# Kernel optimization log

Measured on AMD Instinct MI355X. Metric: run time of the kernel, lower is better.

The kernel has to match this reference:

```python
import jax, jax.numpy as jnp
import numpy as np

N = 50000      # nodes
F_IN = 128     # input features
H = 128        # hidden channels
C = 2          # num classes
E = 1600000    # edges
EPS = 1e-5     # BatchNorm eps


def setup_inputs() -> dict:
    key = jax.random.key(0)
    ks = jax.random.split(key, 4)
    x = jax.random.normal(ks[0], (N, F_IN), dtype=jnp.float32)
    edge_index = jax.random.randint(ks[1], (2, E), 0, N, dtype=jnp.int64)
    W1 = jax.random.normal(ks[2], (F_IN, H), dtype=jnp.float32) * 0.05
    W2 = jax.random.normal(ks[3], (H, C), dtype=jnp.float32) * 0.05
    return {
        "x": x, "edge_index": edge_index,
        "bn0_gamma": jnp.ones((F_IN,), jnp.float32), "bn0_beta": jnp.zeros((F_IN,), jnp.float32),
        "bn0_mean": jnp.zeros((F_IN,), jnp.float32), "bn0_var": jnp.ones((F_IN,), jnp.float32),
        "W1": W1, "b1": jnp.zeros((H,), jnp.float32),
        "bn1_gamma": jnp.ones((H,), jnp.float32), "bn1_beta": jnp.zeros((H,), jnp.float32),
        "bn1_mean": jnp.zeros((H,), jnp.float32), "bn1_var": jnp.ones((H,), jnp.float32),
        "W2": W2, "b2": jnp.zeros((C,), jnp.float32),
    }


def batch_norm_eval(x, gamma, beta, mean, var):
    # BatchNorm over nodes, eval mode: use running stats
    return (x - mean) * jax.lax.rsqrt(var + EPS) * gamma + beta


def gcn_conv(x, edge_index, W, b):
    # GCNConv: x @ W, add self-loops, symmetric deg^{-1/2} normalization, scatter-add
    n = x.shape[0]
    xw = x @ W  # [N, out]
    loop = jnp.arange(n, dtype=edge_index.dtype)
    src = jnp.concatenate([edge_index[0], loop])
    dst = jnp.concatenate([edge_index[1], loop])
    deg = jax.ops.segment_sum(jnp.ones_like(dst, dtype=x.dtype), dst, num_segments=n)
    dinv = jnp.where(deg > 0, jax.lax.rsqrt(jnp.maximum(deg, 1.0)), 0.0)
    norm = dinv[src] * dinv[dst]  # [E+N]
    out = jax.ops.segment_sum(xw[src] * norm[:, None], dst, num_segments=n)
    return out + b


def reference(x, edge_index, bn0_gamma, bn0_beta, bn0_mean, bn0_var,
              W1, b1, bn1_gamma, bn1_beta, bn1_mean, bn1_var, W2, b2):
    # Eval mode: dropout / dropout_edge are identity
    h = batch_norm_eval(x, bn0_gamma, bn0_beta, bn0_mean, bn0_var)
    h = gcn_conv(h, edge_index, W1, b1)
    h = batch_norm_eval(h, bn1_gamma, bn1_beta, bn1_mean, bn1_var)
    h = jax.nn.relu(h)
    return gcn_conv(h, edge_index, W2, b2)
```

## Files before the change

kernel.cpp:

```cpp
#include <hip/hip_runtime.h>

#define EPS 1e-5f
#define CAP 128
#define DR  128
#define NB  391
#define CB  4608
#define GS  16
#define CHUNK 4096

typedef __attribute__((ext_vector_type(8))) short bf16x8;
typedef __attribute__((ext_vector_type(4))) float f32x4;

__device__ __forceinline__ unsigned int f2bf(float f) {
  union { float f; unsigned int u; } v; v.f = f;
  return (v.u + 0x7fffu + ((v.u >> 16) & 1u)) >> 16;
}
__device__ __forceinline__ float bf2f_lo(unsigned int u) {
  union { unsigned int i; float f; } v; v.i = u << 16; return v.f;
}
__device__ __forceinline__ float bf2f_hi(unsigned int u) {
  union { unsigned int i; float f; } v; v.i = u & 0xffff0000u; return v.f;
}

__global__ __launch_bounds__(256) void k_A(
    const int* __restrict__ esrc, const int* __restrict__ edst,
    int* __restrict__ gcur, unsigned int* __restrict__ coarse, int e, int nb_p1,
    const float* __restrict__ W1, const float* __restrict__ b1,
    const float* __restrict__ g0, const float* __restrict__ be0,
    const float* __restrict__ m0, const float* __restrict__ v0,
    const float* __restrict__ g1, const float* __restrict__ be1,
    const float* __restrict__ m1, const float* __restrict__ v1,
    const float4* __restrict__ x,
    unsigned short* __restrict__ Wb, float* __restrict__ c1,
    float* __restrict__ s1, float* __restrict__ u1,
    float* __restrict__ dinv, unsigned short* __restrict__ xsb,
    uint2* __restrict__ Xb4, int n, int n4, int npad4) {
  __shared__ int hist[NB];
  __shared__ int base[NB];
  __shared__ int loff[NB];
  __shared__ float s0s[128], t0s[128];
  const int tid = threadIdx.x;
  int bid = blockIdx.x;
  if (bid < nb_p1) {
    for (int i = tid; i < NB; i += 256) { hist[i] = 0; loff[i] = 0; }
    __syncthreads();
    int e0 = bid * CHUNK;
    int e1 = min(e0 + CHUNK, e);
    for (int i = e0 + tid; i < e1; i += 256)
      atomicAdd(&hist[edst[i] >> 7], 1);
    __syncthreads();
    int rot = bid % NB;
    for (int bb = tid; bb < NB; bb += 256) {
      int b = bb + rot; if (b >= NB) b -= NB;
      int h = hist[b];
      if (h > 0) base[b] = atomicAdd(&gcur[b * GS], h);
    }
    __syncthreads();
    for (int i = e0 + tid; i < e1; i += 256) {
      int d = edst[i], s = esrc[i];
      int b = d >> 7;
      int p = base[b] + atomicAdd(&loff[b], 1);
      if (p < CB) coarse[(size_t)b * CB + p] = ((unsigned int)(d & 127) << 16) | (unsigned int)s;
    }
    return;
  }
  if (bid == nb_p1) {
    if (tid < 128) {
      float s0 = g0[tid] * rsqrtf(v0[tid] + EPS);
      s0s[tid] = s0;
      t0s[tid] = be0[tid] - m0[tid] * s0;
      float s = g1[tid] * rsqrtf(v1[tid] + EPS);
      s1[tid] = s;
      u1[tid] = fmaf(b1[tid] - m1[tid], s, be1[tid]);
    }
    __syncthreads();
    if (tid < 128) {
      float acc = 0.f;
      for (int k = 0; k < 128; ++k) acc = fmaf(t0s[k], W1[k * 128 + tid], acc);
      c1[tid] = acc;
    }
    if (tid == 0) dinv[n] = 0.f;
    if (tid < 16) ((uint4*)xsb)[(size_t)n * 16 + tid] = make_uint4(0, 0, 0, 0);
    for (int idx = tid; idx < 16384; idx += 256) {
      int k = idx >> 7, col = idx & 127;
      float w = W1[idx] * s0s[k];
      int c = k >> 5, j = k & 7, lq2 = (k >> 3) & 3;
      int t = col >> 4, li = col & 15;
      Wb[(((c * 8 + t) * 64) + lq2 * 16 + li) * 8 + j] = (unsigned short)f2bf(w);
    }
    return;
  }
  int i = (bid - nb_p1 - 1) * 256 + tid;
  if (i >= npad4) return;
  uint2 o = make_uint2(0u, 0u);
  if (i < n4) {
    float4 v = x[i];
    o.x = (f2bf(v.y) << 16) | f2bf(v.x);
    o.y = (f2bf(v.w) << 16) | f2bf(v.z);
  }
  Xb4[i] = o;
}

__global__ __launch_bounds__(256) void k_B(
    const int* __restrict__ gcur, const unsigned int* __restrict__ coarse,
    unsigned short* __restrict__ slot, int* __restrict__ wcnt, float* __restrict__ dinv,
    const unsigned short* __restrict__ Xb, const unsigned short* __restrict__ Wb,
    const float* __restrict__ c1, unsigned short* __restrict__ xsb, int n) {
  __shared__ int lcnt[DR];
  __shared__ int nqr[DR];
  __shared__ unsigned short lslot[DR * CAP];
  const int tid = threadIdx.x;
  if (blockIdx.x < NB) {
    for (int i = tid; i < DR; i += 256) lcnt[i] = 0;
    unsigned int padpat = ((unsigned int)n << 16) | (unsigned int)n;
    for (int q = tid; q < DR * CAP / 2; q += 256) ((unsigned int*)lslot)[q] = padpat;
    __syncthreads();
    int cb = blockIdx.x;
    int cnt = gcur[cb * GS]; if (cnt > CB) cnt = CB;
    const unsigned int* src = coarse + (size_t)cb * CB;
    for (int i = tid; i < cnt; i += 256) {
      unsigned int v = src[i];
      int ld = (int)(v >> 16);
      int pos = atomicAdd(&lcnt[ld], 1);
      if (pos < CAP) lslot[ld * CAP + pos] = (unsigned short)(v & 0xffffu);
    }
    __syncthreads();
    int dbase = cb * DR;
    for (int ld = tid; ld < DR; ld += 256) {
      int c = min(lcnt[ld], CAP);
      nqr[ld] = ((((c + 3) >> 2) + 3) & ~3);
      int d = dbase + ld;
      if (d < n) {
        wcnt[d] = c;
        dinv[d] = rsqrtf((float)c + 1.0f);
      }
    }
    __syncthreads();
    const uint2* ls8 = (const uint2*)lslot;
    uint2* s8 = (uint2*)slot;
    for (int idx = tid; idx < DR * 32; idx += 256) {
      int ld = idx >> 5, qi = idx & 31;
      if (qi < nqr[ld] && dbase + ld < n) s8[(size_t)cb * (DR * 32) + idx] = ls8[idx];
    }
    return;
  }
  const int gb = blockIdx.x - NB;
  const int wave = tid >> 6, lane = tid & 63;
  const int r0 = gb * 64 + wave * 16;
  const int lr = lane & 15, lq = lane >> 4;
  const bf16x8* a_base = (const bf16x8*)(Xb + (size_t)(r0 + lr) * 128);
  const bf16x8* wb = (const bf16x8*)Wb;
  f32x4 acc[8];
#pragma unroll
  for (int t = 0; t < 8; ++t) acc[t] = (f32x4){0.f, 0.f, 0.f, 0.f};
#pragma unroll
  for (int c = 0; c < 4; ++c) {
    bf16x8 a = a_base[c * 4 + lq];
#pragma unroll
    for (int t = 0; t < 8; ++t) {
      bf16x8 b = wb[(c * 8 + t) * 64 + lane];
      acc[t] = __builtin_amdgcn_mfma_f32_16x16x32_bf16(a, b, acc[t], 0, 0, 0);
    }
  }
#pragma unroll
  for (int reg = 0; reg < 4; ++reg) {
    int row = r0 + lq * 4 + reg;
    if (row < n) {
      unsigned short* orow = xsb + (size_t)row * 128 + lr;
#pragma unroll
      for (int t = 0; t < 8; ++t) {
        float v = acc[t][reg] + c1[t * 16 + lr];
        orow[t * 16] = (unsigned short)f2bf(v);
      }
    }
  }
}

__global__ __launch_bounds__(256) void k_gather1(const int* __restrict__ wcnt,
                                                 const unsigned short* __restrict__ slot,
                                                 const uint4* __restrict__ xs4,
                                                 const float* __restrict__ dinv,
                                                 const float* __restrict__ s1,
                                                 const float* __restrict__ u1,
                                                 const float* __restrict__ W2,
                                                 float* __restrict__ xs2, int n) {
  int wave = threadIdx.x >> 6, lane = threadIdx.x & 63;
  int d = blockIdx.x * 4 + wave;
  if (d >= n) return;
  int sub = lane >> 4, cl = lane & 15;
  int cnt = wcnt[d];
  int nq4 = ((((cnt + 3) >> 2) + 3) & ~3);
  const unsigned short* slotd = slot + ((size_t)d << 7);
  float a0 = 0.f, a1 = 0.f, a2 = 0.f, a3 = 0.f, a4 = 0.f, a5 = 0.f, a6 = 0.f, a7 = 0.f;
#define ACCF(R, DV) { a0 = fmaf(DV, bf2f_lo(R.x), a0); a1 = fmaf(DV, bf2f_hi(R.x), a1); \
                      a2 = fmaf(DV, bf2f_lo(R.y), a2); a3 = fmaf(DV, bf2f_hi(R.y), a3); \
                      a4 = fmaf(DV, bf2f_lo(R.z), a4); a5 = fmaf(DV, bf2f_hi(R.z), a5); \
                      a6 = fmaf(DV, bf2f_lo(R.w), a6); a7 = fmaf(DV, bf2f_hi(R.w), a7); }
  for (int q = 0; q < nq4; q += 4) {
    int i0 = slotd[(q + 0) * 4 + sub];
    int i1 = slotd[(q + 1) * 4 + sub];
    int i2 = slotd[(q + 2) * 4 + sub];
    int i3 = slotd[(q + 3) * 4 + sub];
    float d0 = dinv[i0], d1 = dinv[i1], d2 = dinv[i2], d3 = dinv[i3];
    uint4 r0 = xs4[(size_t)i0 * 16 + cl];
    uint4 r1 = xs4[(size_t)i1 * 16 + cl];
    uint4 r2 = xs4[(size_t)i2 * 16 + cl];
    uint4 r3 = xs4[(size_t)i3 * 16 + cl];
    ACCF(r0, d0); ACCF(r1, d1); ACCF(r2, d2); ACCF(r3, d3);
  }
#define FOLD(OFF) { a0 += __shfl_xor(a0, OFF); a1 += __shfl_xor(a1, OFF); \
                    a2 += __shfl_xor(a2, OFF); a3 += __shfl_xor(a3, OFF); \
                    a4 += __shfl_xor(a4, OFF); a5 += __shfl_xor(a5, OFF); \
                    a6 += __shfl_xor(a6, OFF); a7 += __shfl_xor(a7, OFF); }
  FOLD(16); FOLD(32);
  float dd = dinv[d];
  uint4 sr = xs4[(size_t)d * 16 + cl];
  ACCF(sr, dd);
#undef ACCF
#undef FOLD
  float4 sA = ((const float4*)s1)[cl * 2], sB = ((const float4*)s1)[cl * 2 + 1];
  float4 uA = ((const float4*)u1)[cl * 2], uB = ((const float4*)u1)[cl * 2 + 1];
  float h0 = fmaxf(fmaf(a0 * dd, sA.x, uA.x), 0.f);
  float h1 = fmaxf(fmaf(a1 * dd, sA.y, uA.y), 0.f);
  float h2 = fmaxf(fmaf(a2 * dd, sA.z, uA.z), 0.f);
  float h3 = fmaxf(fmaf(a3 * dd, sA.w, uA.w), 0.f);
  float h4 = fmaxf(fmaf(a4 * dd, sB.x, uB.x), 0.f);
  float h5 = fmaxf(fmaf(a5 * dd, sB.y, uB.y), 0.f);
  float h6 = fmaxf(fmaf(a6 * dd, sB.z, uB.z), 0.f);
  float h7 = fmaxf(fmaf(a7 * dd, sB.w, uB.w), 0.f);
  float4 wA = ((const float4*)W2)[cl * 4 + 0];
  float4 wB = ((const float4*)W2)[cl * 4 + 1];
  float4 wC = ((const float4*)W2)[cl * 4 + 2];
  float4 wD = ((const float4*)W2)[cl * 4 + 3];
  float p0 = h0 * wA.x + h1 * wA.z + h2 * wB.x + h3 * wB.z
           + h4 * wC.x + h5 * wC.z + h6 * wD.x + h7 * wD.z;
  float p1 = h0 * wA.y + h1 * wA.w + h2 * wB.y + h3 * wB.w
           + h4 * wC.y + h5 * wC.w + h6 * wD.y + h7 * wD.w;
  for (int off = 1; off < 16; off <<= 1) {
    p0 += __shfl_xor(p0, off);
    p1 += __shfl_xor(p1, off);
  }
  if (lane == 0) ((float2*)xs2)[d] = make_float2(p0 * dd, p1 * dd);
}

__global__ __launch_bounds__(256) void k_gather2(const int* __restrict__ wcnt,
                                                 const unsigned short* __restrict__ slot,
                                                 const float* __restrict__ xs2,
                                                 const float* __restrict__ dinv,
                                                 const float* __restrict__ b2,
                                                 float* __restrict__ out, int n) {
  int wave = threadIdx.x >> 6, lane = threadIdx.x & 63;
  int d = blockIdx.x * 4 + wave;
  if (d >= n) return;
  int cnt = wcnt[d];
  const unsigned short* slotd = slot + ((size_t)d << 7);
  float p0 = 0.f, p1 = 0.f;
  for (int k = lane; k < cnt; k += 64) {
    int s = slotd[k];
    float2 v = ((const float2*)xs2)[s];
    p0 += v.x; p1 += v.y;
  }
  for (int off = 32; off > 0; off >>= 1) {
    p0 += __shfl_down(p0, off);
    p1 += __shfl_down(p1, off);
  }
  if (lane == 0) {
    float dd = dinv[d];
    float2 self = ((const float2*)xs2)[d];
    out[d * 2 + 0] = fmaf(dd, p0 + self.x, b2[0]);
    out[d * 2 + 1] = fmaf(dd, p1 + self.y, b2[1]);
  }
}

extern "C" void kernel_launch(void* const* d_in, const int* in_sizes, int n_in,
                              void* d_out, int out_size, void* d_ws, size_t ws_size,
                              hipStream_t stream) {
  const float* x   = (const float*)d_in[0];
  const int*   ei  = (const int*)d_in[1];
  const float* g0  = (const float*)d_in[2];
  const float* be0 = (const float*)d_in[3];
  const float* m0  = (const float*)d_in[4];
  const float* v0  = (const float*)d_in[5];
  const float* W1  = (const float*)d_in[6];
  const float* b1  = (const float*)d_in[7];
  const float* g1  = (const float*)d_in[8];
  const float* be1 = (const float*)d_in[9];
  const float* m1  = (const float*)d_in[10];
  const float* v1  = (const float*)d_in[11];
  const float* W2  = (const float*)d_in[12];
  const float* b2  = (const float*)d_in[13];
  float* out = (float*)d_out;

  const int n = in_sizes[0] / 128;
  const int e = in_sizes[1] / 2;
  const int* esrc = ei;
  const int* edst = ei + e;
  const int npad = ((n + 63) / 64) * 64;

  int*            gcur   = (int*)d_ws;
  unsigned int*   coarse = (unsigned int*)(gcur + 6272);
  unsigned short* slot   = (unsigned short*)(coarse + (size_t)NB * CB);
  int*            wcnt   = (int*)(slot + (size_t)n * CAP);
  float*          dinv   = (float*)(wcnt + n);
  unsigned short* Wb     = (unsigned short*)(dinv + n + 4);
  float*          c1     = (float*)(Wb + 16384);
  float*          s1     = c1 + 128;
  float*          u1     = s1 + 128;
  float*          xs2    = u1 + 128;
  unsigned short* Xb     = (unsigned short*)(xs2 + (size_t)n * 2);
  unsigned short* xsb    = Xb + (size_t)npad * 128;

  const int nb_p1 = (e + CHUNK - 1) / CHUNK;
  const int cvb   = (npad * 32 + 255) / 256;
  hipMemsetAsync(gcur, 0, NB * GS * sizeof(int), stream);
  k_A<<<nb_p1 + 1 + cvb, 256, 0, stream>>>(esrc, edst, gcur, coarse, e, nb_p1,
                                           W1, b1, g0, be0, m0, v0, g1, be1, m1, v1,
                                           (const float4*)x, Wb, c1, s1, u1, dinv, xsb,
                                           (uint2*)Xb, n, n * 32, npad * 32);
  k_B<<<NB + npad / 64, 256, 0, stream>>>(gcur, coarse, slot, wcnt, dinv, Xb, Wb, c1, xsb, n);
  k_gather1<<<(n + 3) / 4, 256, 0, stream>>>(wcnt, slot, (const uint4*)xsb, dinv, s1, u1, W2, xs2, n);
  k_gather2<<<(n + 3) / 4, 256, 0, stream>>>(wcnt, slot, xs2, dinv, b2, out, n);
}
```

Baseline: 215.1 us.

## Fuse all GCN stages into one cooperative persistent kernel with grid syncs

Replaces the memset and four separate kernel launches with a single cooperative kernel. The stages are separated by grid.sync, and work is distributed in grid-stride loops over a persistent grid sized from occupancy. It also adds a pass that prescales the bf16 hidden features by dinv, so the gather no longer loads dinv per neighbour, at the cost of an extra read-write sweep and a second bf16 rounding. The aim is to remove launch gaps and per-edge dinv loads. The risks are grid-sync overhead and lower parallelism in the gather stages, since the grid is limited to resident blocks.

```diff
diff --git a/kernel.cpp b/kernel.cpp
--- a/kernel.cpp
+++ b/kernel.cpp
@@ -1,4 +1,5 @@
 #include <hip/hip_runtime.h>
+#include <hip/hip_cooperative_groups.h>
 
 #define EPS 1e-5f
 #define CAP 128
@@ -22,279 +23,270 @@
   union { unsigned int i; float f; } v; v.i = u & 0xffff0000u; return v.f;
 }
 
-__global__ __launch_bounds__(256) void k_A(
-    const int* __restrict__ esrc, const int* __restrict__ edst,
-    int* __restrict__ gcur, unsigned int* __restrict__ coarse, int e, int nb_p1,
-    const float* __restrict__ W1, const float* __restrict__ b1,
-    const float* __restrict__ g0, const float* __restrict__ be0,
-    const float* __restrict__ m0, const float* __restrict__ v0,
-    const float* __restrict__ g1, const float* __restrict__ be1,
-    const float* __restrict__ m1, const float* __restrict__ v1,
-    const float4* __restrict__ x,
-    unsigned short* __restrict__ Wb, float* __restrict__ c1,
-    float* __restrict__ s1, float* __restrict__ u1,
-    float* __restrict__ dinv, unsigned short* __restrict__ xsb,
-    uint2* __restrict__ Xb4, int n, int n4, int npad4) {
-  __shared__ int hist[NB];
-  __shared__ int base[NB];
-  __shared__ int loff[NB];
-  __shared__ float s0s[128], t0s[128];
+struct Params {
+  const int *esrc, *edst;
+  const float4* x;
+  const float *W1, *b1, *g0, *be0, *m0, *v0, *g1, *be1, *m1, *v1, *W2, *b2;
+  int* gcur; unsigned int* coarse; unsigned short* slot; int* wcnt; float* dinv;
+  unsigned short* Wb; float *c1, *s1, *u1, *xs2;
+  unsigned short *Xb, *xsb;
+  float* out;
+  int n, e, npad, nbp1;
+};
+
+__global__ __launch_bounds__(256, 4) void k_fused(Params P) {
+  namespace cg = cooperative_groups;
+  cg::grid_group grid = cg::this_grid();
+  __shared__ int SM[8448];
   const int tid = threadIdx.x;
-  int bid = blockIdx.x;
-  if (bid < nb_p1) {
-    for (int i = tid; i < NB; i += 256) { hist[i] = 0; loff[i] = 0; }
-    __syncthreads();
-    int e0 = bid * CHUNK;
-    int e1 = min(e0 + CHUNK, e);
-    for (int i = e0 + tid; i < e1; i += 256)
-      atomicAdd(&hist[edst[i] >> 7], 1);
-    __syncthreads();
-    int rot = bid % NB;
-    for (int bb = tid; bb < NB; bb += 256) {
-      int b = bb + rot; if (b >= NB) b -= NB;
-      int h = hist[b];
-      if (h > 0) base[b] = atomicAdd(&gcur[b * GS], h);
-    }
-    __syncthreads();
-    for (int i = e0 + tid; i < e1; i += 256) {
-      int d = edst[i], s = esrc[i];
-      int b = d >> 7;
-      int p = base[b] + atomicAdd(&loff[b], 1);
-      if (p < CB) coarse[(size_t)b * CB + p] = ((unsigned int)(d & 127) << 16) | (unsigned int)s;
-    }
-    return;
-  }
-  if (bid == nb_p1) {
-    if (tid < 128) {
-      float s0 = g0[tid] * rsqrtf(v0[tid] + EPS);
-      s0s[tid] = s0;
-      t0s[tid] = be0[tid] - m0[tid] * s0;
-      float s = g1[tid] * rsqrtf(v1[tid] + EPS);
-      s1[tid] = s;
-      u1[tid] = fmaf(b1[tid] - m1[tid], s, be1[tid]);
-    }
-    __syncthreads();
-    if (tid < 128) {
-      float acc = 0.f;
-      for (int k = 0; k < 128; ++k) acc = fmaf(t0s[k], W1[k * 128 + tid], acc);
-      c1[tid] = acc;
-    }
-    if (tid == 0) dinv[n] = 0.f;
-    if (tid < 16) ((uint4*)xsb)[(size_t)n * 16 + tid] = make_uint4(0, 0, 0, 0);
-    for (int idx = tid; idx < 16384; idx += 256) {
-      int k = idx >> 7, col = idx & 127;
-      float w = W1[idx] * s0s[k];
-      int c = k >> 5, j = k & 7, lq2 = (k >> 3) & 3;
-      int t = col >> 4, li = col & 15;
-      Wb[(((c * 8 + t) * 64) + lq2 * 16 + li) * 8 + j] = (unsigned short)f2bf(w);
-    }
-    return;
-  }
-  int i = (bid - nb_p1 - 1) * 256 + tid;
-  if (i >= npad4) return;
-  uint2 o = make_uint2(0u, 0u);
-  if (i < n4) {
-    float4 v = x[i];
-    o.x = (f2bf(v.y) << 16) | f2bf(v.x);
-    o.y = (f2bf(v.w) << 16) | f2bf(v.z);
-  }
-  Xb4[i] = o;
-}
-
-__global__ __launch_bounds__(256) void k_B(
-    const int* __restrict__ gcur, const unsigned int* __restrict__ coarse,
-    unsigned short* __restrict__ slot, int* __restrict__ wcnt, float* __restrict__ dinv,
-    const unsigned short* __restrict__ Xb, const unsigned short* __restrict__ Wb,
-    const float* __restrict__ c1, unsigned short* __restrict__ xsb, int n) {
-  __shared__ int lcnt[DR];
-  __shared__ int nqr[DR];
-  __shared__ unsigned short lslot[DR * CAP];
-  const int tid = threadIdx.x;
-  if (blockIdx.x < NB) {
-    for (int i = tid; i < DR; i += 256) lcnt[i] = 0;
-    unsigned int padpat = ((unsigned int)n << 16) | (unsigned int)n;
-    for (int q = tid; q < DR * CAP / 2; q += 256) ((unsigned int*)lslot)[q] = padpat;
-    __syncthreads();
-    int cb = blockIdx.x;
-    int cnt = gcur[cb * GS]; if (cnt > CB) cnt = CB;
-    const unsigned int* src = coarse + (size_t)cb * CB;
-    for (int i = tid; i < cnt; i += 256) {
-      unsigned int v = src[i];
-      int ld = (int)(v >> 16);
-      int pos = atomicAdd(&lcnt[ld], 1);
-      if (pos < CAP) lslot[ld * CAP + pos] = (unsigned short)(v & 0xffffu);
-    }
-    __syncthreads();
-    int dbase = cb * DR;
-    for (int ld = tid; ld < DR; ld += 256) {
-      int c = min(lcnt[ld], CAP);
-      nqr[ld] = ((((c + 3) >> 2) + 3) & ~3);
-      int d = dbase + ld;
-      if (d < n) {
-        wcnt[d] = c;
-        dinv[d] = rsqrtf((float)c + 1.0f);
-      }
-    }
-    __syncthreads();
-    const uint2* ls8 = (const uint2*)lslot;
-    uint2* s8 = (uint2*)slot;
-    for (int idx = tid; idx < DR * 32; idx += 256) {
-      int ld = idx >> 5, qi = idx & 31;
-      if (qi < nqr[ld] && dbase + ld < n) s8[(size_t)cb * (DR * 32) + idx] = ls8[idx];
-    }
-    return;
-  }
-  const int gb = blockIdx.x - NB;
-  const int wave = tid >> 6, lane = tid & 63;
-  const int r0 = gb * 64 + wave * 16;
-  const int lr = lane & 15, lq = lane >> 4;
-  const bf16x8* a_base = (const bf16x8*)(Xb + (size_t)(r0 + lr) * 128);
-  const bf16x8* wb = (const bf16x8*)Wb;
-  f32x4 acc[8];
-#pragma unroll
-  for (int t = 0; t < 8; ++t) acc[t] = (f32x4){0.f, 0.f, 0.f, 0.f};
-#pragma unroll
-  for (int c = 0; c < 4; ++c) {
-    bf16x8 a = a_base[c * 4 + lq];
-#pragma unroll
-    for (int t = 0; t < 8; ++t) {
-      bf16x8 b = wb[(c * 8 + t) * 64 + lane];
-      acc[t] = __builtin_amdgcn_mfma_f32_16x16x32_bf16(a, b, acc[t], 0, 0, 0);
-    }
-  }
-#pragma unroll
-  for (int reg = 0; reg < 4; ++reg) {
-    int row = r0 + lq * 4 + reg;
-    if (row < n) {
-      unsigned short* orow = xsb + (size_t)row * 128 + lr;
-#pragma unroll
-      for (int t = 0; t < 8; ++t) {
-        float v = acc[t][reg] + c1[t * 16 + lr];
-        orow[t * 16] = (unsigned short)f2bf(v);
-      }
-    }
-  }
-}
-
-__global__ __launch_bounds__(256) void k_gather1(const int* __restrict__ wcnt,
-                                                 const unsigned short* __restrict__ slot,
-                                                 const uint4* __restrict__ xs4,
-                                                 const float* __restrict__ dinv,
-                                                 const float* __restrict__ s1,
-                                                 const float* __restrict__ u1,
-                                                 const float* __restrict__ W2,
-                                                 float* __restrict__ xs2, int n) {
-  int wave = threadIdx.x >> 6, lane = threadIdx.x & 63;
-  int d = blockIdx.x * 4 + wave;
-  if (d >= n) return;
-  int sub = lane >> 4, cl = lane & 15;
-  int cnt = wcnt[d];
-  int nq4 = ((((cnt + 3) >> 2) + 3) & ~3);
-  const unsigned short* slotd = slot + ((size_t)d << 7);
-  float a0 = 0.f, a1 = 0.f, a2 = 0.f, a3 = 0.f, a4 = 0.f, a5 = 0.f, a6 = 0.f, a7 = 0.f;
-#define ACCF(R, DV) { a0 = fmaf(DV, bf2f_lo(R.x), a0); a1 = fmaf(DV, bf2f_hi(R.x), a1); \
-                      a2 = fmaf(DV, bf2f_lo(R.y), a2); a3 = fmaf(DV, bf2f_hi(R.y), a3); \
-                      a4 = fmaf(DV, bf2f_lo(R.z), a4); a5 = fmaf(DV, bf2f_hi(R.z), a5); \
-                      a6 = fmaf(DV, bf2f_lo(R.w), a6); a7 = fmaf(DV, bf2f_hi(R.w), a7); }
-  for (int q = 0; q < nq4; q += 4) {
-    int i0 = slotd[(q + 0) * 4 + sub];
-    int i1 = slotd[(q + 1) * 4 + sub];
-    int i2 = slotd[(q + 2) * 4 + sub];
-    int i3 = slotd[(q + 3) * 4 + sub];
-    float d0 = dinv[i0], d1 = dinv[i1], d2 = dinv[i2], d3 = dinv[i3];
-    uint4 r0 = xs4[(size_t)i0 * 16 + cl];
-    uint4 r1 = xs4[(size_t)i1 * 16 + cl];
-    uint4 r2 = xs4[(size_t)i2 * 16 + cl];
-    uint4 r3 = xs4[(size_t)i3 * 16 + cl];
-    ACCF(r0, d0); ACCF(r1, d1); ACCF(r2, d2); ACCF(r3, d3);
-  }
+  const int nblk = gridDim.x;
+  const int gtid = blockIdx.x * 256 + tid;
+  const int gstride = nblk * 256;
+
+  for (int i = gtid; i < NB * GS; i += gstride) P.gcur[i] = 0;
+  grid.sync();
+
+  {
+    int n4 = P.n * 32, npad4 = P.npad * 32;
+    for (int i = gtid; i < npad4; i += gstride) {
+      uint2 o = make_uint2(0u, 0u);
+      if (i < n4) {
+        float4 v = P.x[i];
+        o.x = (f2bf(v.y) << 16) | f2bf(v.x);
+        o.y = (f2bf(v.w) << 16) | f2bf(v.z);
+      }
+      ((uint2*)P.Xb)[i] = o;
+    }
+    for (int wb = blockIdx.x; wb < P.nbp1 + 1; wb += nblk) {
+      if (wb < P.nbp1) {
+        int* hist = SM; int* base = SM + NB; int* loff = SM + 2 * NB;
+        for (int i = tid; i < NB; i += 256) { hist[i] = 0; loff[i] = 0; }
+        __syncthreads();
+        int e0 = wb * CHUNK, e1 = min(e0 + CHUNK, P.e);
+        for (int i = e0 + tid; i < e1; i += 256) atomicAdd(&hist[P.edst[i] >> 7], 1);
+        __syncthreads();
+        int rot = wb % NB;
+        for (int bb = tid; bb < NB; bb += 256) {
+          int b = bb + rot; if (b >= NB) b -= NB;
+          int h = hist[b];
+          if (h > 0) base[b] = atomicAdd(&P.gcur[b * GS], h);
+        }
+        __syncthreads();
+        for (int i = e0 + tid; i < e1; i += 256) {
+          int d = P.edst[i], s = P.esrc[i];
+          int b = d >> 7;
+          int p = base[b] + atomicAdd(&loff[b], 1);
+          if (p < CB) P.coarse[(size_t)b * CB + p] = ((unsigned)(d & 127) << 16) | (unsigned)s;
+        }
+      } else {
+        float* s0s = (float*)SM; float* t0s = s0s + 128;
+        if (tid < 128) {
+          float s0 = P.g0[tid] * rsqrtf(P.v0[tid] + EPS);
+          s0s[tid] = s0;
+          t0s[tid] = P.be0[tid] - P.m0[tid] * s0;
+          float s = P.g1[tid] * rsqrtf(P.v1[tid] + EPS);
+          P.s1[tid] = s;
+          P.u1[tid] = fmaf(P.b1[tid] - P.m1[tid], s, P.be1[tid]);
+        }
+        __syncthreads();
+        if (tid < 128) {
+          float acc = 0.f;
+          for (int k = 0; k < 128; ++k) acc = fmaf(t0s[k], P.W1[k * 128 + tid], acc);
+          P.c1[tid] = acc;
+        }
+        if (tid == 0) P.dinv[P.n] = 0.f;
+        if (tid < 16) ((uint4*)P.xsb)[(size_t)P.n * 16 + tid] = make_uint4(0, 0, 0, 0);
+        for (int idx = tid; idx < 16384; idx += 256) {
+          int k = idx >> 7, col = idx & 127;
+          float w = P.W1[idx] * s0s[k];
+          int c = k >> 5, j = k & 7, lq2 = (k >> 3) & 3;
+          int t = col >> 4, li = col & 15;
+          P.Wb[(((c * 8 + t) * 64) + lq2 * 16 + li) * 8 + j] = (unsigned short)f2bf(w);
+        }
+      }
+      __syncthreads();
+    }
+  }
+  grid.sync();
+
+  {
+    int ngemm = P.npad / 64;
+    for (int wb = blockIdx.x; wb < NB + ngemm; wb += nblk) {
+      if (wb < NB) {
+        int* lcnt = SM; int* nqr = SM + 128;
+        unsigned short* lslot = (unsigned short*)(SM + 256);
+        for (int i = tid; i < DR; i += 256) lcnt[i] = 0;
+        unsigned pad2 = ((unsigned)P.n << 16) | (unsigned)P.n;
+        for (int q = tid; q < DR * CAP / 2; q += 256) ((unsigned*)lslot)[q] = pad2;
+        __syncthreads();
+        int cb = wb;
+        int cnt = P.gcur[cb * GS]; if (cnt > CB) cnt = CB;
+        const unsigned* src = P.coarse + (size_t)cb * CB;
+        for (int i = tid; i < cnt; i += 256) {
+          unsigned v = src[i];
+          int ld = (int)(v >> 16);
+          int pos = atomicAdd(&lcnt[ld], 1);
+          if (pos < CAP) lslot[ld * CAP + pos] = (unsigned short)(v & 0xffffu);
+        }
+        __syncthreads();
+        int dbase = cb * DR;
+        for (int ld = tid; ld < DR; ld += 256) {
+          int c = min(lcnt[ld], CAP);
+          nqr[ld] = ((((c + 3) >> 2) + 3) & ~3);
+          int d = dbase + ld;
+          if (d < P.n) { P.wcnt[d] = c; P.dinv[d] = rsqrtf((float)c + 1.0f); }
+        }
+        __syncthreads();
+        const uint2* ls8 = (const uint2*)lslot;
+        uint2* s8 = (uint2*)P.slot;
+        for (int idx = tid; idx < DR * 32; idx += 256) {
+          int ld = idx >> 5, qi = idx & 31;
+          if (qi < nqr[ld] && dbase + ld < P.n) s8[(size_t)cb * (DR * 32) + idx] = ls8[idx];
+        }
+      } else {
+        int gb = wb - NB;
+        const int wave = tid >> 6, lane = tid & 63;
+        int r0 = gb * 64 + wave * 16;
+        int lr = lane & 15, lq = lane >> 4;
+        const bf16x8* a_base = (const bf16x8*)(P.Xb + (size_t)(r0 + lr) * 128);
+        const bf16x8* wbp = (const bf16x8*)P.Wb;
+        f32x4 acc[8];
+#pragma unroll
+        for (int t = 0; t < 8; ++t) acc[t] = (f32x4){0.f, 0.f, 0.f, 0.f};
+#pragma unroll
+        for (int c = 0; c < 4; ++c) {
+          bf16x8 a = a_base[c * 4 + lq];
+#pragma unroll
+          for (int t = 0; t < 8; ++t) {
+            bf16x8 b = wbp[(c * 8 + t) * 64 + lane];
+            acc[t] = __builtin_amdgcn_mfma_f32_16x16x32_bf16(a, b, acc[t], 0, 0, 0);
+          }
+        }
+#pragma unroll
+        for (int reg = 0; reg < 4; ++reg) {
+          int row = r0 + lq * 4 + reg;
+          if (row < P.n) {
+            unsigned short* orow = P.xsb + (size_t)row * 128 + lr;
+#pragma unroll
+            for (int t = 0; t < 8; ++t) {
+              float v = acc[t][reg] + P.c1[t * 16 + lr];
+              orow[t * 16] = (unsigned short)f2bf(v);
+            }
+          }
+        }
+      }
+      __syncthreads();
+    }
+  }
+  grid.sync();
+
+  {
+    uint4* xb4 = (uint4*)P.xsb;
+    int total = P.n * 16;
+    for (int i = gtid; i < total; i += gstride) {
+      float dd = P.dinv[i >> 4];
+      uint4 v = xb4[i];
+      v.x = (f2bf(bf2f_hi(v.x) * dd) << 16) | f2bf(bf2f_lo(v.x) * dd);
+      v.y = (f2bf(bf2f_hi(v.y) * dd) << 16) | f2bf(bf2f_lo(v.y) * dd);
+      v.z = (f2bf(bf2f_hi(v.z) * dd) << 16) | f2bf(bf2f_lo(v.z) * dd);
+      v.w = (f2bf(bf2f_hi(v.w) * dd) << 16) | f2bf(bf2f_lo(v.w) * dd);
+      xb4[i] = v;
+    }
+  }
+  grid.sync();
+
+  {
+    const int wave = tid >> 6, lane = tid & 63;
+    const int sub = lane >> 4, cl = lane & 15;
+    const uint4* xs4 = (const uint4*)P.xsb;
+    float4 sA = ((const float4*)P.s1)[cl * 2], sB = ((const float4*)P.s1)[cl * 2 + 1];
+    float4 uA = ((const float4*)P.u1)[cl * 2], uB = ((const float4*)P.u1)[cl * 2 + 1];
+    float4 wA = ((const float4*)P.W2)[cl * 4 + 0];
+    float4 wB = ((const float4*)P.W2)[cl * 4 + 1];
+    float4 wC = ((const float4*)P.W2)[cl * 4 + 2];
+    float4 wD = ((const float4*)P.W2)[cl * 4 + 3];
+    int nwaves = nblk * 4;
+    for (int d = blockIdx.x * 4 + wave; d < P.n; d += nwaves) {
+      int cnt = P.wcnt[d];
+      int nq4 = ((((cnt + 3) >> 2) + 3) & ~3);
+      const unsigned short* slotd = P.slot + ((size_t)d << 7);
+      float a0 = 0.f, a1 = 0.f, a2 = 0.f, a3 = 0.f, a4 = 0.f, a5 = 0.f, a6 = 0.f, a7 = 0.f;
+#define ACC(R) { a0 += bf2f_lo(R.x); a1 += bf2f_hi(R.x); a2 += bf2f_lo(R.y); a3 += bf2f_hi(R.y); \
+                 a4 += bf2f_lo(R.z); a5 += bf2f_hi(R.z); a6 += bf2f_lo(R.w); a7 += bf2f_hi(R.w); }
+      for (int q = 0; q < nq4; q += 4) {
+        int i0 = slotd[(q + 0) * 4 + sub];
+        int i1 = slotd[(q + 1) * 4 + sub];
+        int i2 = slotd[(q + 2) * 4 + sub];
+        int i3 = slotd[(q + 3) * 4 + sub];
+        uint4 r0 = xs4[(size_t)i0 * 16 + cl];
+        uint4 r1 = xs4[(size_t)i1 * 16 + cl];
+        uint4 r2 = xs4[(size_t)i2 * 16 + cl];
+        uint4 r3 = xs4[(size_t)i3 * 16 + cl];
+        ACC(r0); ACC(r1); ACC(r2); ACC(r3);
+      }
 #define FOLD(OFF) { a0 += __shfl_xor(a0, OFF); a1 += __shfl_xor(a1, OFF); \
                     a2 += __shfl_xor(a2, OFF); a3 += __shfl_xor(a3, OFF); \
                     a4 += __shfl_xor(a4, OFF); a5 += __shfl_xor(a5, OFF); \
                     a6 += __shfl_xor(a6, OFF); a7 += __shfl_xor(a7, OFF); }
-  FOLD(16); FOLD(32);
-  float dd = dinv[d];
-  uint4 sr = xs4[(size_t)d * 16 + cl];
-  ACCF(sr, dd);
-#undef ACCF
+      FOLD(16); FOLD(32);
+      uint4 sr = xs4[(size_t)d * 16 + cl];
+      ACC(sr);
+#undef ACC
 #undef FOLD
-  float4 sA = ((const float4*)s1)[cl * 2], sB = ((const float4*)s1)[cl * 2 + 1];
-  float4 uA = ((const float4*)u1)[cl * 2], uB = ((const float4*)u1)[cl * 2 + 1];
-  float h0 = fmaxf(fmaf(a0 * dd, sA.x, uA.x), 0.f);
-  float h1 = fmaxf(fmaf(a1 * dd, sA.y, uA.y), 0.f);
-  float h2 = fmaxf(fmaf(a2 * dd, sA.z, uA.z), 0.f);
-  float h3 = fmaxf(fmaf(a3 * dd, sA.w, uA.w), 0.f);
-  float h4 = fmaxf(fmaf(a4 * dd, sB.x, uB.x), 0.f);
-  float h5 = fmaxf(fmaf(a5 * dd, sB.y, uB.y), 0.f);
-  float h6 = fmaxf(fmaf(a6 * dd, sB.z, uB.z), 0.f);
-  float h7 = fmaxf(fmaf(a7 * dd, sB.w, uB.w), 0.f);
-  float4 wA = ((const float4*)W2)[cl * 4 + 0];
-  float4 wB = ((const float4*)W2)[cl * 4 + 1];
-  float4 wC = ((const float4*)W2)[cl * 4 + 2];
-  float4 wD = ((const float4*)W2)[cl * 4 + 3];
-  float p0 = h0 * wA.x + h1 * wA.z + h2 * wB.x + h3 * wB.z
-           + h4 * wC.x + h5 * wC.z + h6 * wD.x + h7 * wD.z;
-  float p1 = h0 * wA.y + h1 * wA.w + h2 * wB.y + h3 * wB.w
-           + h4 * wC.y + h5 * wC.w + h6 * wD.y + h7 * wD.w;
-  for (int off = 1; off < 16; off <<= 1) {
-    p0 += __shfl_xor(p0, off);
-    p1 += __shfl_xor(p1, off);
-  }
-  if (lane == 0) ((float2*)xs2)[d] = make_float2(p0 * dd, p1 * dd);
-}
-
-__global__ __launch_bounds__(256) void k_gather2(const int* __restrict__ wcnt,
-                                                 const unsigned short* __restrict__ slot,
-                                                 const float* __restrict__ xs2,
-                                                 const float* __restrict__ dinv,
-                                                 const float* __restrict__ b2,
-                                                 float* __restrict__ out, int n) {
-  int wave = threadIdx.x >> 6, lane = threadIdx.x & 63;
-  int d = blockIdx.x * 4 + wave;
-  if (d >= n) return;
-  int cnt = wcnt[d];
-  const unsigned short* slotd = slot + ((size_t)d << 7);
-  float p0 = 0.f, p1 = 0.f;
-  for (int k = lane; k < cnt; k += 64) {
-    int s = slotd[k];
-    float2 v = ((const float2*)xs2)[s];
-    p0 += v.x; p1 += v.y;
-  }
-  for (int off = 32; off > 0; off >>= 1) {
-    p0 += __shfl_down(p0, off);
-    p1 += __shfl_down(p1, off);
-  }
-  if (lane == 0) {
-    float dd = dinv[d];
-    float2 self = ((const float2*)xs2)[d];
-    out[d * 2 + 0] = fmaf(dd, p0 + self.x, b2[0]);
-    out[d * 2 + 1] = fmaf(dd, p1 + self.y, b2[1]);
+      float dd = P.dinv[d];
+      float h0 = fmaxf(fmaf(a0 * dd, sA.x, uA.x), 0.f);
+      float h1 = fmaxf(fmaf(a1 * dd, sA.y, uA.y), 0.f);
+      float h2 = fmaxf(fmaf(a2 * dd, sA.z, uA.z), 0.f);
+      float h3 = fmaxf(fmaf(a3 * dd, sA.w, uA.w), 0.f);
+      float h4 = fmaxf(fmaf(a4 * dd, sB.x, uB.x), 0.f);
+      float h5 = fmaxf(fmaf(a5 * dd, sB.y, uB.y), 0.f);
+      float h6 = fmaxf(fmaf(a6 * dd, sB.z, uB.z), 0.f);
+      float h7 = fmaxf(fmaf(a7 * dd, sB.w, uB.w), 0.f);
+      float p0 = h0 * wA.x + h1 * wA.z + h2 * wB.x + h3 * wB.z
+               + h4 * wC.x + h5 * wC.z + h6 * wD.x + h7 * wD.z;
+      float p1 = h0 * wA.y + h1 * wA.w + h2 * wB.y + h3 * wB.w
+               + h4 * wC.y + h5 * wC.w + h6 * wD.y + h7 * wD.w;
+      for (int off = 1; off < 16; off <<= 1) {
+        p0 += __shfl_xor(p0, off);
+        p1 += __shfl_xor(p1, off);
+      }
+      if (lane == 0) ((float2*)P.xs2)[d] = make_float2(p0 * dd, p1 * dd);
+    }
+  }
+  grid.sync();
+
+  {
+    const int wave = tid >> 6, lane = tid & 63;
+    float b20 = P.b2[0], b21 = P.b2[1];
+    int nwaves = nblk * 4;
+    for (int d = blockIdx.x * 4 + wave; d < P.n; d += nwaves) {
+      int cnt = P.wcnt[d];
+      const unsigned short* slotd = P.slot + ((size_t)d << 7);
+      float p0 = 0.f, p1 = 0.f;
+      for (int k = lane; k < cnt; k += 64) {
+        int s = slotd[k];
+        float2 v = ((const float2*)P.xs2)[s];
+        p0 += v.x; p1 += v.y;
+      }
+      for (int off = 32; off > 0; off >>= 1) {
+        p0 += __shfl_down(p0, off);
+        p1 += __shfl_down(p1, off);
+      }
+      if (lane == 0) {
+        float dd = P.dinv[d];
+        float2 self = ((const float2*)P.xs2)[d];
+        P.out[d * 2 + 0] = fmaf(dd, p0 + self.x, b20);
+        P.out[d * 2 + 1] = fmaf(dd, p1 + self.y, b21);
+      }
+    }
   }
 }
 
 extern "C" void kernel_launch(void* const* d_in, const int* in_sizes, int n_in,
                               void* d_out, int out_size, void* d_ws, size_t ws_size,
                               hipStream_t stream) {
-  const float* x   = (const float*)d_in[0];
-  const int*   ei  = (const int*)d_in[1];
-  const float* g0  = (const float*)d_in[2];
-  const float* be0 = (const float*)d_in[3];
-  const float* m0  = (const float*)d_in[4];
-  const float* v0  = (const float*)d_in[5];
-  const float* W1  = (const float*)d_in[6];
-  const float* b1  = (const float*)d_in[7];
-  const float* g1  = (const float*)d_in[8];
-  const float* be1 = (const float*)d_in[9];
-  const float* m1  = (const float*)d_in[10];
-  const float* v1  = (const float*)d_in[11];
-  const float* W2  = (const float*)d_in[12];
-  const float* b2  = (const float*)d_in[13];
-  float* out = (float*)d_out;
-
   const int n = in_sizes[0] / 128;
   const int e = in_sizes[1] / 2;
-  const int* esrc = ei;
-  const int* edst = ei + e;
   const int npad = ((n + 63) / 64) * 64;
 
   int*            gcur   = (int*)d_ws;
@@ -310,14 +302,35 @@
   unsigned short* Xb     = (unsigned short*)(xs2 + (size_t)n * 2);
   unsigned short* xsb    = Xb + (size_t)npad * 128;
 
-  const int nb_p1 = (e + CHUNK - 1) / CHUNK;
-  const int cvb   = (npad * 32 + 255) / 256;
-  hipMemsetAsync(gcur, 0, NB * GS * sizeof(int), stream);
-  k_A<<<nb_p1 + 1 + cvb, 256, 0, stream>>>(esrc, edst, gcur, coarse, e, nb_p1,
-                                           W1, b1, g0, be0, m0, v0, g1, be1, m1, v1,
-                                           (const float4*)x, Wb, c1, s1, u1, dinv, xsb,
-                                           (uint2*)Xb, n, n * 32, npad * 32);
-  k_B<<<NB + npad / 64, 256, 0, stream>>>(gcur, coarse, slot, wcnt, dinv, Xb, Wb, c1, xsb, n);
-  k_gather1<<<(n + 3) / 4, 256, 0, stream>>>(wcnt, slot, (const uint4*)xsb, dinv, s1, u1, W2, xs2, n);
-  k_gather2<<<(n + 3) / 4, 256, 0, stream>>>(wcnt, slot, xs2, dinv, b2, out, n);
-}
+  Params prm;
+  prm.esrc = (const int*)d_in[1];
+  prm.edst = ((const int*)d_in[1]) + e;
+  prm.x   = (const float4*)d_in[0];
+  prm.W1  = (const float*)d_in[6];  prm.b1  = (const float*)d_in[7];
+  prm.g0  = (const float*)d_in[2];  prm.be0 = (const float*)d_in[3];
+  prm.m0  = (const float*)d_in[4];  prm.v0  = (const float*)d_in[5];
+  prm.g1  = (const float*)d_in[8];  prm.be1 = (const float*)d_in[9];
+  prm.m1  = (const float*)d_in[10]; prm.v1  = (const float*)d_in[11];
+  prm.W2  = (const float*)d_in[12]; prm.b2  = (const float*)d_in[13];
+  prm.gcur = gcur; prm.coarse = coarse; prm.slot = slot; prm.wcnt = wcnt; prm.dinv = dinv;
+  prm.Wb = Wb; prm.c1 = c1; prm.s1 = s1; prm.u1 = u1; prm.xs2 = xs2;
+  prm.Xb = Xb; prm.xsb = xsb;
+  prm.out = (float*)d_out;
+  prm.n = n; prm.e = e; prm.npad = npad;
+  prm.nbp1 = (e + CHUNK - 1) / CHUNK;
+
+  int nbPerCU = 0;
+  (void)hipOccupancyMaxActiveBlocksPerMultiprocessor(&nbPerCU, k_fused, 256, 0);
+  if (nbPerCU < 1) nbPerCU = 1;
+  int dev = 0, cus = 0;
+  (void)hipGetDevice(&dev);
+  (void)hipDeviceGetAttribute(&cus, hipDeviceAttributeMultiprocessorCount, dev);
+  if (cus <= 0) cus = 256;
+  long long nblocks = (long long)nbPerCU * cus;
+  if (nblocks > 2048) nblocks = 2048;
+  if (nblocks < 64) nblocks = 64;
+
+  void* args[] = { (void*)&prm };
+  (void)hipLaunchCooperativeKernel((const void*)k_fused, dim3((unsigned)nblocks), dim3(256),
+                                   args, 0, stream);
+}
```

New measurement: 591.0 us. +174.7%, slower.

## Prescale layer-1 features by source dinv, drop per-edge dinv gathers

Applied to the files above, without the earlier changes.

Each edge's destination degree is now counted with global atomics in k_A, into a padded per-node counter array (one int per 32-int stride). The k_B GEMM epilogue then multiplies each transformed row by its own deg^-1/2 before writing bf16 features. The first gather can therefore sum the neighbour rows directly, with no per-edge dinv loads or multiplies. The cost is 1.6M extra global atomics, a memset of about 6.4 MB, and dinv[n] is no longer zeroed, which the second gather may still rely on for padding slots.

```diff
diff --git a/kernel.cpp b/kernel.cpp
--- a/kernel.cpp
+++ b/kernel.cpp
@@ -6,6 +6,7 @@
 #define NB  391
 #define CB  4608
 #define GS  16
+#define CS  32
 #define CHUNK 4096
 
 typedef __attribute__((ext_vector_type(8))) short bf16x8;
@@ -24,7 +25,8 @@
 
 __global__ __launch_bounds__(256) void k_A(
     const int* __restrict__ esrc, const int* __restrict__ edst,
-    int* __restrict__ gcur, unsigned int* __restrict__ coarse, int e, int nb_p1,
+    int* __restrict__ gcur, int* __restrict__ cntp,
+    unsigned int* __restrict__ coarse, int e, int nb_p1,
     const float* __restrict__ W1, const float* __restrict__ b1,
     const float* __restrict__ g0, const float* __restrict__ be0,
     const float* __restrict__ m0, const float* __restrict__ v0,
@@ -33,7 +35,7 @@
     const float4* __restrict__ x,
     unsigned short* __restrict__ Wb, float* __restrict__ c1,
     float* __restrict__ s1, float* __restrict__ u1,
-    float* __restrict__ dinv, unsigned short* __restrict__ xsb,
+    unsigned short* __restrict__ xsb,
     uint2* __restrict__ Xb4, int n, int n4, int npad4) {
   __shared__ int hist[NB];
   __shared__ int base[NB];
@@ -46,8 +48,11 @@
     __syncthreads();
     int e0 = bid * CHUNK;
     int e1 = min(e0 + CHUNK, e);
-    for (int i = e0 + tid; i < e1; i += 256)
-      atomicAdd(&hist[edst[i] >> 7], 1);
+    for (int i = e0 + tid; i < e1; i += 256) {
+      int d = edst[i];
+      atomicAdd(&hist[d >> 7], 1);
+      atomicAdd(&cntp[d << 5], 1);
+    }
     __syncthreads();
     int rot = bid % NB;
     for (int bb = tid; bb < NB; bb += 256) {
@@ -79,7 +84,6 @@
       for (int k = 0; k < 128; ++k) acc = fmaf(t0s[k], W1[k * 128 + tid], acc);
       c1[tid] = acc;
     }
-    if (tid == 0) dinv[n] = 0.f;
     if (tid < 16) ((uint4*)xsb)[(size_t)n * 16 + tid] = make_uint4(0, 0, 0, 0);
     for (int idx = tid; idx < 16384; idx += 256) {
       int k = idx >> 7, col = idx & 127;
@@ -102,7 +106,8 @@
 }
 
 __global__ __launch_bounds__(256) void k_B(
-    const int* __restrict__ gcur, const unsigned int* __restrict__ coarse,
+    const int* __restrict__ gcur, const int* __restrict__ cntp,
+    const unsigned int* __restrict__ coarse,
     unsigned short* __restrict__ slot, int* __restrict__ wcnt, float* __restrict__ dinv,
     const unsigned short* __restrict__ Xb, const unsigned short* __restrict__ Wb,
     const float* __restrict__ c1, unsigned short* __restrict__ xsb, int n) {
@@ -166,10 +171,11 @@
   for (int reg = 0; reg < 4; ++reg) {
     int row = r0 + lq * 4 + reg;
     if (row < n) {
+      float dd = rsqrtf((float)min(cntp[row << 5], CAP) + 1.0f);
       unsigned short* orow = xsb + (size_t)row * 128 + lr;
 #pragma unroll
       for (int t = 0; t < 8; ++t) {
-        float v = acc[t][reg] + c1[t * 16 + lr];
+        float v = (acc[t][reg] + c1[t * 16 + lr]) * dd;
         orow[t * 16] = (unsigned short)f2bf(v);
       }
     }
@@ -192,32 +198,29 @@
   int nq4 = ((((cnt + 3) >> 2) + 3) & ~3);
   const unsigned short* slotd = slot + ((size_t)d << 7);
   float a0 = 0.f, a1 = 0.f, a2 = 0.f, a3 = 0.f, a4 = 0.f, a5 = 0.f, a6 = 0.f, a7 = 0.f;
-#define ACCF(R, DV) { a0 = fmaf(DV, bf2f_lo(R.x), a0); a1 = fmaf(DV, bf2f_hi(R.x), a1); \
-                      a2 = fmaf(DV, bf2f_lo(R.y), a2); a3 = fmaf(DV, bf2f_hi(R.y), a3); \
-                      a4 = fmaf(DV, bf2f_lo(R.z), a4); a5 = fmaf(DV, bf2f_hi(R.z), a5); \
-                      a6 = fmaf(DV, bf2f_lo(R.w), a6); a7 = fmaf(DV, bf2f_hi(R.w), a7); }
+#define ACC(R) { a0 += bf2f_lo(R.x); a1 += bf2f_hi(R.x); a2 += bf2f_lo(R.y); a3 += bf2f_hi(R.y); \
+                 a4 += bf2f_lo(R.z); a5 += bf2f_hi(R.z); a6 += bf2f_lo(R.w); a7 += bf2f_hi(R.w); }
   for (int q = 0; q < nq4; q += 4) {
     int i0 = slotd[(q + 0) * 4 + sub];
     int i1 = slotd[(q + 1) * 4 + sub];
     int i2 = slotd[(q + 2) * 4 + sub];
     int i3 = slotd[(q + 3) * 4 + sub];
-    float d0 = dinv[i0], d1 = dinv[i1], d2 = dinv[i2], d3 = dinv[i3];
     uint4 r0 = xs4[(size_t)i0 * 16 + cl];
     uint4 r1 = xs4[(size_t)i1 * 16 + cl];
     uint4 r2 = xs4[(size_t)i2 * 16 + cl];
     uint4 r3 = xs4[(size_t)i3 * 16 + cl];
-    ACCF(r0, d0); ACCF(r1, d1); ACCF(r2, d2); ACCF(r3, d3);
+    ACC(r0); ACC(r1); ACC(r2); ACC(r3);
   }
 #define FOLD(OFF) { a0 += __shfl_xor(a0, OFF); a1 += __shfl_xor(a1, OFF); \
                     a2 += __shfl_xor(a2, OFF); a3 += __shfl_xor(a3, OFF); \
                     a4 += __shfl_xor(a4, OFF); a5 += __shfl_xor(a5, OFF); \
                     a6 += __shfl_xor(a6, OFF); a7 += __shfl_xor(a7, OFF); }
   FOLD(16); FOLD(32);
+  uint4 sr = xs4[(size_t)d * 16 + cl];
+  ACC(sr);
+#undef ACC
+#undef FOLD
   float dd = dinv[d];
-  uint4 sr = xs4[(size_t)d * 16 + cl];
-  ACCF(sr, dd);
-#undef ACCF
-#undef FOLD
   float4 sA = ((const float4*)s1)[cl * 2], sB = ((const float4*)s1)[cl * 2 + 1];
   float4 uA = ((const float4*)u1)[cl * 2], uB = ((const float4*)u1)[cl * 2 + 1];
   float h0 = fmaxf(fmaf(a0 * dd, sA.x, uA.x), 0.f);
@@ -298,11 +301,12 @@
   const int npad = ((n + 63) / 64) * 64;
 
   int*            gcur   = (int*)d_ws;
-  unsigned int*   coarse = (unsigned int*)(gcur + 6272);
+  int*            cntp   = gcur + 6272;
+  unsigned int*   coarse = (unsigned int*)(cntp + (size_t)n * CS);
   unsigned short* slot   = (unsigned short*)(coarse + (size_t)NB * CB);
   int*            wcnt   = (int*)(slot + (size_t)n * CAP);
   float*          dinv   = (float*)(wcnt + n);
-  unsigned short* Wb     = (unsigned short*)(dinv + n + 4);
+  unsigned short* Wb     = (unsigned short*)(dinv + n);
   float*          c1     = (float*)(Wb + 16384);
   float*          s1     = c1 + 128;
   float*          u1     = s1 + 128;
@@ -312,12 +316,13 @@
 
   const int nb_p1 = (e + CHUNK - 1) / CHUNK;
   const int cvb   = (npad * 32 + 255) / 256;
-  hipMemsetAsync(gcur, 0, NB * GS * sizeof(int), stream);
-  k_A<<<nb_p1 + 1 + cvb, 256, 0, stream>>>(esrc, edst, gcur, coarse, e, nb_p1,
+  hipMemsetAsync(gcur, 0, (6272 + (size_t)n * CS) * sizeof(int), stream);
+  k_A<<<nb_p1 + 1 + cvb, 256, 0, stream>>>(esrc, edst, gcur, cntp, coarse, e, nb_p1,
                                            W1, b1, g0, be0, m0, v0, g1, be1, m1, v1,
-                                           (const float4*)x, Wb, c1, s1, u1, dinv, xsb,
+                                           (const float4*)x, Wb, c1, s1, u1, xsb,
                                            (uint2*)Xb, n, n * 32, npad * 32);
-  k_B<<<NB + npad / 64, 256, 0, stream>>>(gcur, coarse, slot, wcnt, dinv, Xb, Wb, c1, xsb, n);
+  k_B<<<NB + npad / 64, 256, 0, stream>>>(gcur, cntp, coarse, slot, wcnt, dinv,
+                                          Xb, Wb, c1, xsb, n);
   k_gather1<<<(n + 3) / 4, 256, 0, stream>>>(wcnt, slot, (const uint4*)xsb, dinv, s1, u1, W2, xs2, n);
   k_gather2<<<(n + 3) / 4, 256, 0, stream>>>(wcnt, slot, xs2, dinv, b2, out, n);
 }
```

Result: slower. 255.6 us (+18.8%).
